# Kernel optimization log

Hardware: AMD Instinct MI355X
Metric: run time of the kernel (lower is better)

The kernel has to match this reference:

```python
import jax, jax.numpy as jnp
import numpy as np

B, T, ENC, TAG, HG, HE, M = 64, 383, 768, 128, 400, 256, 20
D = ENC + TAG          # graph RNN input size (encoder_output_dim + tag_representation_dim)
S = T + 1              # +1 for head sentinel


def setup_inputs() -> dict:
    ks = jax.random.split(jax.random.key(0), 16)
    g = lambda i, shape, s=0.05: jax.random.normal(ks[i], shape, dtype=jnp.float32) * s
    z = lambda n: jnp.zeros((n,), jnp.float32)
    return dict(
        input=g(0, (B, T, ENC), 1.0),
        tag_embeddings=g(1, (B, T, TAG), 1.0),
        mask=jnp.ones((B, T), jnp.int32),
        head_sentinel=g(2, (D,), 1.0),
        # bidirectional graph RNN (tanh, 1 layer)
        Wih_f=g(3, (HG, D)), Whh_f=g(4, (HG, HG)), bih_f=z(HG), bhh_f=z(HG),
        Wih_b=g(5, (HG, D)), Whh_b=g(6, (HG, HG)), bih_b=z(HG), bhh_b=z(HG),
        # graph_to_edge projection (edge RNN initial hidden)
        Wg2e=g(7, (HE, 2 * HG)), bg2e=z(HE),
        # edge RNN (past direction, input size 1) + edge classifier head
        Wih_e=g(8, (HE, 1)), Whh_e=g(9, (HE, HE)), bih_e=z(HE), bhh_e=z(HE),
        Wcls=g(10, (1, HE)), bcls=z(1),
        bos=z(1),
        # head/dep tag feedforwards
        Wht=g(11, (TAG, 2 * HG)), bht=z(TAG),
        Wdt=g(12, (TAG, 2 * HG)), bdt=z(TAG),
    )


def _masked_rnn(x, m, Wih, Whh, bih, bhh, reverse):
    # x: [B,S,D], m: [B,S,1]. Emulates packed nn.RNN(tanh) for one direction:
    # hidden only advances on valid steps (so the backward direction starts its
    # recurrence at each sequence's true length), outputs are zero on padding
    # (matching pad_packed_sequence zero padding).
    def step(h, inp):
        xt, mt = inp
        hn = jnp.tanh(xt @ Wih.T + bih + h @ Whh.T + bhh)
        h = mt * hn + (1.0 - mt) * h
        return h, h * mt

    h0 = jnp.zeros((x.shape[0], Wih.shape[0]), x.dtype)
    _, ys = jax.lax.scan(step, h0, (x.swapaxes(0, 1), m.swapaxes(0, 1)), reverse=reverse)
    return ys.swapaxes(0, 1)


def reference(input, tag_embeddings, mask, head_sentinel,
              Wih_f, Whh_f, bih_f, bhh_f, Wih_b, Whh_b, bih_b, bhh_b,
              Wg2e, bg2e, Wih_e, Whh_e, bih_e, bhh_e, Wcls, bcls, bos,
              Wht, bht, Wdt, bdt):
    x = jnp.concatenate([input, tag_embeddings], axis=-1)            # [B,T,D]
    sent = jnp.broadcast_to(head_sentinel, (B, 1, D))
    x = jnp.concatenate([sent, x], axis=1)                           # [B,S,D]
    m = jnp.concatenate([jnp.ones((B, 1), mask.dtype), mask], axis=1)  # sentinel is valid
    mf = m.astype(x.dtype)[..., None]                                # [B,S,1]

    fwd = _masked_rnn(x, mf, Wih_f, Whh_f, bih_f, bhh_f, reverse=False)
    bwd = _masked_rnn(x, mf, Wih_b, Whh_b, bih_b, bhh_b, reverse=True)
    graph_state = jnp.concatenate([fwd, bwd], axis=-1)               # [B,S,2*HG]

    # initial hidden = graph_to_edge(graph_state), input starts at bos, then
    # feeds back the previous logit.
    proj = graph_state.reshape(B * S, 2 * HG) @ Wg2e.T + bg2e        # [B*S,HE]
    steps = min(M, S)
    x0 = jnp.broadcast_to(bos.reshape(1, 1), (B * S, 1))

    def estep(carry, _):
        xe, h = carry
        hn = jnp.tanh(xe @ Wih_e.T + bih_e + h @ Whh_e.T + bhh_e)
        logit = hn @ Wcls.T + bcls                                   # [B*S,1]
        return (logit, hn), logit

    _, logits = jax.lax.scan(estep, (x0, proj), None, length=steps)  # [steps,B*S,1]
    Ap = logits.squeeze(-1).T.reshape(B, S, steps)                   # [B,S,steps]

    # banded scatter: arc_logits[:, i, start:i] = Ap[:, i, :i-start], start=max(0,i-M)
    rows = jnp.arange(S)[:, None]
    cols = jnp.arange(S)[None, :]
    start = jnp.maximum(0, rows - M)
    k = cols - start
    valid = (cols >= start) & (cols < rows)
    idx = jnp.clip(k, 0, steps - 1)
    band = Ap[:, jnp.broadcast_to(rows, (S, S)), jnp.broadcast_to(idx, (S, S))]  # [B,S,S]
    arc_logits = jnp.where(valid[None], band, jnp.zeros((), Ap.dtype))

    # tag feedforwards (Dropout is identity in eval)
    head_tag = jax.nn.elu(graph_state @ Wht.T + bht)
    dep_tag = jax.nn.elu(graph_state @ Wdt.T + bdt)
    return head_tag, dep_tag, arc_logits
```

## Files before the change

kernel.cpp:

```cpp
#include <hip/hip_runtime.h>

#define B_ 64
#define T_ 383
#define S_ 384
#define ENC_ 768
#define TAGD_ 128
#define D_ 896
#define HG_ 400
#define HE_ 256
#define MSTEP_ 20
#define RTOT_ (B_*S_)
#define HEAD_SZ_ ((size_t)RTOT_*TAGD_)

typedef short short8 __attribute__((ext_vector_type(8)));
typedef float f32x4 __attribute__((ext_vector_type(4)));

__device__ __forceinline__ float bf2f(unsigned short u){
  union { unsigned int i; float f; } v; v.i = ((unsigned int)u) << 16; return v.f;
}
__device__ __forceinline__ unsigned short f2bf(float f){
  union { float f; unsigned int i; } v; v.f = f;
  unsigned int r = (v.i + 0x7fffu + ((v.i >> 16) & 1u)) >> 16;
  return (unsigned short)r;
}
__device__ __forceinline__ float tanh_fast(float x){
  float xc = fminf(fmaxf(x, -15.f), 15.f);
  float e = __expf(2.f*xc);
  return (e - 1.f) * __builtin_amdgcn_rcpf(e + 1.f);
}

__device__ __forceinline__ void probe_maps(int lane, int* mlab, int* nlab){
  unsigned short lb = f2bf((float)(lane & 15));
  short8 av, bv;
  #pragma unroll
  for (int j = 0; j < 8; j++){ av[j] = (short)lb; bv[j] = (short)0x3F80; }
  f32x4 z = {0.f,0.f,0.f,0.f};
  f32x4 d1 = __builtin_amdgcn_mfma_f32_16x16x32_bf16(av, bv, z, 0, 0, 0);
  f32x4 d2 = __builtin_amdgcn_mfma_f32_16x16x32_bf16(bv, av, z, 0, 0, 0);
  #pragma unroll
  for (int i = 0; i < 4; i++){
    mlab[i] = (int)(d1[i]*0.03125f + 0.5f);
    nlab[i] = (int)(d2[i]*0.03125f + 0.5f);
  }
}

__global__ __launch_bounds__(256) void cvt4(const float* __restrict__ src,
                                            unsigned short* __restrict__ dst, int n4)
{
  int i = blockIdx.x*256 + threadIdx.x;
  if (i >= n4) return;
  float4 v = ((const float4*)src)[i];
  ((ushort4*)dst)[i] = make_ushort4(f2bf(v.x), f2bf(v.y), f2bf(v.z), f2bf(v.w));
}

__global__ __launch_bounds__(256) void pack_wrnn3(const float* __restrict__ Wf,
                                                  const float* __restrict__ Wb,
                                                  unsigned short* __restrict__ Wr)
{
  int idx = blockIdx.x*256 + threadIdx.x;
  if (idx >= 2*26*13*16*32) return;
  int dir = idx / (26*13*16*32);
  int rem = idx % (26*13*16*32);
  int tile = rem / (13*16*32); rem %= (13*16*32);
  int kt = rem / (16*32);      rem %= (16*32);
  int r  = rem / 32;
  int kk = rem % 32;
  int n = tile*16 + r, k = kt*32 + kk;
  unsigned short v = 0;
  if (n < HG_ && k < HG_) v = f2bf((dir ? Wb : Wf)[(size_t)n*HG_ + k]);
  Wr[idx] = v;
}

__global__ __launch_bounds__(64) void maskpack(const int* __restrict__ mask,
                                               unsigned long long* __restrict__ mb)
{
  int t = blockIdx.x; int b = threadIdx.x;
  int m = (t > 0) ? mask[b*T_ + (t-1)] : 1;
  unsigned long long v = __ballot(m != 0);
  if (b == 0) mb[t] = v;
}

__global__ __launch_bounds__(256) void gemm_pre(
    const float* __restrict__ inp, const float* __restrict__ tag,
    const float* __restrict__ sent, const unsigned short* __restrict__ W,
    const float* __restrict__ bihf, const float* __restrict__ bhhf,
    const float* __restrict__ bihb, const float* __restrict__ bhhb,
    unsigned short* __restrict__ preT2)
{
  int wid = blockIdx.x*4 + (threadIdx.x >> 6);
  int lane = threadIdx.x & 63;
  int q = lane >> 4, l16 = lane & 15;
  int mt = wid / 25, ct = wid % 25;
  int r = mt*16 + l16;
  int s = r % S_, b = r / S_;
  int mlab[4], nlab[4];
  probe_maps(lane, mlab, nlab);
  int n0 = ct*32 + l16, n1 = n0 + 16;
  const unsigned short* w0 = W + (size_t)n0*D_;
  const unsigned short* w1 = W + (size_t)n1*D_;
  f32x4 acc0 = {0.f,0.f,0.f,0.f}, acc1 = {0.f,0.f,0.f,0.f};
  for (int k0 = 0; k0 < D_; k0 += 32){
    int k = k0 + q*8;
    const float* asrc = (s == 0) ? (sent + k)
        : ((k < ENC_) ? inp + (size_t)(b*T_ + (s-1))*ENC_ + k
                      : tag + (size_t)(b*T_ + (s-1))*TAGD_ + (k - ENC_));
    float4 v0 = *(const float4*)asrc;
    float4 v1 = *(const float4*)(asrc + 4);
    union { unsigned int u[4]; short8 s8; } au;
    asm("v_cvt_pk_bf16_f32 %0, %1, %2" : "=v"(au.u[0]) : "v"(v0.x), "v"(v0.y));
    asm("v_cvt_pk_bf16_f32 %0, %1, %2" : "=v"(au.u[1]) : "v"(v0.z), "v"(v0.w));
    asm("v_cvt_pk_bf16_f32 %0, %1, %2" : "=v"(au.u[2]) : "v"(v1.x), "v"(v1.y));
    asm("v_cvt_pk_bf16_f32 %0, %1, %2" : "=v"(au.u[3]) : "v"(v1.z), "v"(v1.w));
    short8 a = au.s8;
    acc0 = __builtin_amdgcn_mfma_f32_16x16x32_bf16(a, *(const short8*)(w0 + k), acc0, 0,0,0);
    acc1 = __builtin_amdgcn_mfma_f32_16x16x32_bf16(a, *(const short8*)(w1 + k), acc1, 0,0,0);
  }
  #pragma unroll
  for (int i = 0; i < 4; i++){
    int row = mt*16 + mlab[i];
    int c0 = ct*32 + nlab[i], c1 = c0 + 16;
    int bb = row / S_, ss = row % S_;
    int mtb = bb >> 4, qb = (bb >> 2) & 3, rib = bb & 3;
    float v0 = acc0[i] + ((c0 < HG_) ? (bihf[c0] + bhhf[c0]) : (bihb[c0-HG_] + bhhb[c0-HG_]));
    float v1 = acc1[i] + ((c1 < HG_) ? (bihf[c1] + bhhf[c1]) : (bihb[c1-HG_] + bhhb[c1-HG_]));
    {
      int d = (c0 >= HG_) ? 1 : 0; int nn = c0 - d*HG_;
      int nt = nn >> 4, lc = nn & 15;
      preT2[((((size_t)(d*S_ + ss)*25 + nt)*4 + mtb)*64 + (qb*16 + lc))*4 + rib] = f2bf(v0);
    }
    {
      int d = (c1 >= HG_) ? 1 : 0; int nn = c1 - d*HG_;
      int nt = nn >> 4, lc = nn & 15;
      preT2[((((size_t)(d*S_ + ss)*25 + nt)*4 + mtb)*64 + (qb*16 + lc))*4 + rib] = f2bf(v1);
    }
  }
}

#define HSTR5_ 424
__device__ __forceinline__ void rnn_epi6(int n, const f32x4& acc, const ushort4& pu,
    unsigned long long mb, bool allm, int bg, int q,
    unsigned short (*Hh)[HSTR5_], unsigned short (*Hl)[HSTR5_])
{
  unsigned short pv[4] = {pu.x, pu.y, pu.z, pu.w};
  #pragma unroll
  for (int ri = 0; ri < 4; ri++){
    int b = q*4 + ri;
    float hn = tanh_fast(acc[ri] + bf2f(pv[ri]));
    float hnew;
    if (allm) hnew = hn;
    else {
      bool mv = (mb >> (bg*16 + b)) & 1ull;
      float hold = bf2f(Hh[b][n]) + bf2f(Hl[b][n]);
      hnew = mv ? hn : hold;
    }
    unsigned short hi = f2bf(hnew);
    Hh[b][n] = hi;
    Hl[b][n] = f2bf(hnew - bf2f(hi));
  }
}

template<bool EXTRA>
__device__ void rnn_body6(int nt0, int dir, int bg, int lane, int tid,
    const unsigned short* __restrict__ pD,
    const unsigned short* __restrict__ Wd,
    const unsigned long long* __restrict__ mbits,
    unsigned short* __restrict__ gs,
    unsigned short (*Hh)[HSTR5_], unsigned short (*Hl)[HSTR5_])
{
  int q = lane >> 4, l16 = lane & 15;

  short8 bh[3][13];
  #pragma unroll
  for (int j = 0; j < 3; j++){
    const unsigned short* wr = Wd + (size_t)(nt0 + j)*13*512 + l16*32 + q*8;
    #pragma unroll
    for (int kt = 0; kt < 13; kt++)
      bh[j][kt] = *(const short8*)(wr + kt*512);
  }
  const unsigned short* wx = Wd + (size_t)24*13*512 + l16*32 + q*8;

  for (int stp = 0; stp < S_; stp++){
    int t = dir ? (S_ - 1 - stp) : stp;
    unsigned long long mb = mbits[t];
    bool allm = (mb == 0xFFFFFFFFFFFFFFFFull);
    const unsigned short* pT = pD + (size_t)t*25600;

    ushort4 pu[3]; ushort4 pux = make_ushort4(0,0,0,0);
    #pragma unroll
    for (int j = 0; j < 3; j++)
      pu[j] = *(const ushort4*)(pT + (((size_t)(nt0 + j)*4 + bg)*64 + lane)*4);
    if (EXTRA)
      pux = *(const ushort4*)(pT + (((size_t)24*4 + bg)*64 + lane)*4);

    f32x4 acc[3]; f32x4 accx = {0.f,0.f,0.f,0.f};
    #pragma unroll
    for (int j = 0; j < 3; j++) acc[j] = (f32x4){0.f,0.f,0.f,0.f};

    #pragma unroll
    for (int kt = 0; kt < 13; kt++){
      short8 ah = *(const short8*)&Hh[l16][kt*32 + q*8];
      short8 al = *(const short8*)&Hl[l16][kt*32 + q*8];
      if (EXTRA){
        short8 bx = *(const short8*)(wx + kt*512);
        accx = __builtin_amdgcn_mfma_f32_16x16x32_bf16(ah, bx, accx, 0,0,0);
        accx = __builtin_amdgcn_mfma_f32_16x16x32_bf16(al, bx, accx, 0,0,0);
      }
      #pragma unroll
      for (int j = 0; j < 3; j++){
        acc[j] = __builtin_amdgcn_mfma_f32_16x16x32_bf16(ah, bh[j][kt], acc[j], 0,0,0);
        acc[j] = __builtin_amdgcn_mfma_f32_16x16x32_bf16(al, bh[j][kt], acc[j], 0,0,0);
      }
    }

    __syncthreads();

    #pragma unroll
    for (int j = 0; j < 3; j++)
      rnn_epi6((nt0 + j)*16 + l16, acc[j], pu[j], mb, allm, bg, q, Hh, Hl);
    if (EXTRA)
      rnn_epi6(24*16 + l16, accx, pux, mb, allm, bg, q, Hh, Hl);

    __syncthreads();

    for (int c = tid; c < 800; c += 512){
      int b = c / 50, off = c - b*50;
      uint4 dv = *(const uint4*)&Hh[b][off*8];
      bool mv = (mb >> (bg*16 + b)) & 1ull;
      uint4 z = make_uint4(0,0,0,0);
      *(uint4*)(gs + (size_t)((bg*16 + b)*S_ + t)*800 + dir*HG_ + off*8) = mv ? dv : z;
    }
  }
}

__global__ __launch_bounds__(512, 1) void rnn_mfma6(
    const unsigned short* __restrict__ preT2, const unsigned short* __restrict__ Wr,
    const unsigned long long* __restrict__ mbits, unsigned short* __restrict__ gs)
{
  __shared__ __align__(16) unsigned short Hh[16][HSTR5_];
  __shared__ __align__(16) unsigned short Hl[16][HSTR5_];
  int tid = threadIdx.x;
  int wave = tid >> 6, lane = tid & 63;
  int dir = blockIdx.x >> 2, bg = blockIdx.x & 3;
  for (int i = tid; i < 16*HSTR5_/2; i += 512){
    ((unsigned int*)Hh)[i] = 0u;
    ((unsigned int*)Hl)[i] = 0u;
  }
  __syncthreads();
  const unsigned short* Wd = Wr + (size_t)dir*26*13*512;
  const unsigned short* pD = preT2 + (size_t)dir*S_*25600;
  if (wave == 0) rnn_body6<true >(0,       dir, bg, lane, tid, pD, Wd, mbits, gs, Hh, Hl);
  else           rnn_body6<false>(wave*3,  dir, bg, lane, tid, pD, Wd, mbits, gs, Hh, Hl);
}

__global__ __launch_bounds__(256) void gemm_proj(
    const unsigned short* __restrict__ gs, const unsigned short* __restrict__ Wg2e,
    const float* __restrict__ bg2e, float* __restrict__ proj)
{
  int wid = blockIdx.x*4 + (threadIdx.x >> 6);
  int lane = threadIdx.x & 63;
  int q = lane >> 4, l16 = lane & 15;
  int mt = wid >> 3, ct = wid & 7;
  int mlab[4], nlab[4];
  probe_maps(lane, mlab, nlab);
  const unsigned short* arow = gs + (size_t)(mt*16 + l16)*800;
  int n0 = ct*32 + l16, n1 = n0 + 16;
  const unsigned short* w0 = Wg2e + (size_t)n0*800;
  const unsigned short* w1 = Wg2e + (size_t)n1*800;
  f32x4 acc0 = {0.f,0.f,0.f,0.f}, acc1 = {0.f,0.f,0.f,0.f};
  for (int k0 = 0; k0 < 800; k0 += 32){
    int k = k0 + q*8;
    short8 a = *(const short8*)(arow + k);
    acc0 = __builtin_amdgcn_mfma_f32_16x16x32_bf16(a, *(const short8*)(w0 + k), acc0, 0,0,0);
    acc1 = __builtin_amdgcn_mfma_f32_16x16x32_bf16(a, *(const short8*)(w1 + k), acc1, 0,0,0);
  }
  #pragma unroll
  for (int i = 0; i < 4; i++){
    int row = mt*16 + mlab[i];
    int c0 = ct*32 + nlab[i], c1 = c0 + 16;
    proj[(size_t)row*HE_ + c0] = acc0[i] + bg2e[c0];
    proj[(size_t)row*HE_ + c1] = acc1[i] + bg2e[c1];
  }
}

__global__ __launch_bounds__(256) void gemm_tag(
    const unsigned short* __restrict__ gs, const unsigned short* __restrict__ Wtag,
    const float* __restrict__ bht, const float* __restrict__ bdt,
    float* __restrict__ outH)
{
  int wid = blockIdx.x*4 + (threadIdx.x >> 6);
  int lane = threadIdx.x & 63;
  int q = lane >> 4, l16 = lane & 15;
  int mt = wid >> 3, ct = wid & 7;
  int mlab[4], nlab[4];
  probe_maps(lane, mlab, nlab);
  const unsigned short* arow = gs + (size_t)(mt*16 + l16)*800;
  int n0 = ct*32 + l16, n1 = n0 + 16;
  const unsigned short* w0 = Wtag + (size_t)n0*800;
  const unsigned short* w1 = Wtag + (size_t)n1*800;
  f32x4 acc0 = {0.f,0.f,0.f,0.f}, acc1 = {0.f,0.f,0.f,0.f};
  for (int k0 = 0; k0 < 800; k0 += 32){
    int k = k0 + q*8;
    short8 a = *(const short8*)(arow + k);
    acc0 = __builtin_amdgcn_mfma_f32_16x16x32_bf16(a, *(const short8*)(w0 + k), acc0, 0,0,0);
    acc1 = __builtin_amdgcn_mfma_f32_16x16x32_bf16(a, *(const short8*)(w1 + k), acc1, 0,0,0);
  }
  #pragma unroll
  for (int i = 0; i < 4; i++){
    int row = mt*16 + mlab[i];
    int c0 = ct*32 + nlab[i], c1 = c0 + 16;
    float v0 = acc0[i] + ((c0 < TAGD_) ? bht[c0] : bdt[c0-TAGD_]);
    float v1 = acc1[i] + ((c1 < TAGD_) ? bht[c1] : bdt[c1-TAGD_]);
    v0 = (v0 > 0.f) ? v0 : expm1f(v0);
    v1 = (v1 > 0.f) ? v1 : expm1f(v1);
    if (c0 < TAGD_) outH[(size_t)row*TAGD_ + c0] = v0;
    else            outH[HEAD_SZ_ + (size_t)row*TAGD_ + (c0-TAGD_)] = v0;
    if (c1 < TAGD_) outH[(size_t)row*TAGD_ + c1] = v1;
    else            outH[HEAD_SZ_ + (size_t)row*TAGD_ + (c1-TAGD_)] = v1;
  }
}

#define EROWS_ 96
#define ESTR_ 264
__global__ __launch_bounds__(256, 1) void estep2(
    const float* __restrict__ proj, const unsigned short* __restrict__ WhhE,
    const float* __restrict__ bihE, const float* __restrict__ bhhE,
    const float* __restrict__ WihE, const float* __restrict__ Wcls,
    const float* __restrict__ bclsp, const float* __restrict__ bosp,
    float* __restrict__ Ap)
{
  __shared__ __align__(16) unsigned short H[2][EROWS_][ESTR_];
  __shared__ float lacc[4][EROWS_];
  __shared__ float xls[EROWS_];
  int tid = threadIdx.x;
  int wave = tid >> 6, lane = tid & 63, q = lane >> 4, l16 = lane & 15;
  size_t rowbase = (size_t)blockIdx.x * EROWS_;

  short8 bw[4][8];
  float bias_n[4], wcl_n[4], wih_n[4];
  #pragma unroll
  for (int nt = 0; nt < 4; nt++){
    int n = wave*64 + nt*16 + l16;
    #pragma unroll
    for (int kt = 0; kt < 8; kt++)
      bw[nt][kt] = *(const short8*)(WhhE + (size_t)n*HE_ + kt*32 + q*8);
    bias_n[nt] = bihE[n] + bhhE[n];
    wcl_n[nt]  = Wcls[n];
    wih_n[nt]  = WihE[n];
  }
  for (int i = tid; i < EROWS_*HE_; i += 256){
    int r = i >> 8, n = i & 255;
    H[0][r][n] = f2bf(proj[(rowbase + r)*HE_ + n]);
  }
  if (tid < EROWS_) xls[tid] = bosp[0];
  float bc = bclsp[0];
  __syncthreads();

  for (int stp = 0; stp < MSTEP_; stp++){
    int cur = stp & 1, nxt = cur ^ 1;
    float lp[6][4];
    #pragma unroll
    for (int mt = 0; mt < 6; mt++){
      short8 af[8];
      #pragma unroll
      for (int kt = 0; kt < 8; kt++)
        af[kt] = *(const short8*)&H[cur][mt*16 + l16][kt*32 + q*8];
      float xr[4];
      #pragma unroll
      for (int ri = 0; ri < 4; ri++) xr[ri] = xls[mt*16 + q*4 + ri];
      f32x4 acc[4];
      #pragma unroll
      for (int nt = 0; nt < 4; nt++) acc[nt] = (f32x4){0.f,0.f,0.f,0.f};
      #pragma unroll
      for (int kt = 0; kt < 8; kt++){
        #pragma unroll
        for (int nt = 0; nt < 4; nt++)
          acc[nt] = __builtin_amdgcn_mfma_f32_16x16x32_bf16(af[kt], bw[nt][kt], acc[nt], 0,0,0);
      }
      #pragma unroll
      for (int ri = 0; ri < 4; ri++) lp[mt][ri] = 0.f;
      #pragma unroll
      for (int nt = 0; nt < 4; nt++){
        int n = wave*64 + nt*16 + l16;
        #pragma unroll
        for (int ri = 0; ri < 4; ri++){
          float v = acc[nt][ri] + bias_n[nt] + xr[ri]*wih_n[nt];
          float h = tanh_fast(v);
          lp[mt][ri] += h * wcl_n[nt];
          H[nxt][mt*16 + q*4 + ri][n] = f2bf(h);
        }
      }
    }
    #pragma unroll
    for (int mt = 0; mt < 6; mt++){
      #pragma unroll
      for (int ri = 0; ri < 4; ri++){
        float v = lp[mt][ri];
        v += __shfl_xor(v, 1, 16);
        v += __shfl_xor(v, 2, 16);
        v += __shfl_xor(v, 4, 16);
        v += __shfl_xor(v, 8, 16);
        lp[mt][ri] = v;
      }
    }
    if (l16 == 0){
      #pragma unroll
      for (int mt = 0; mt < 6; mt++)
        #pragma unroll
        for (int ri = 0; ri < 4; ri++)
          lacc[wave][mt*16 + q*4 + ri] = lp[mt][ri];
    }
    __syncthreads();
    if (tid < EROWS_){
      float lg = lacc[0][tid] + lacc[1][tid] + lacc[2][tid] + lacc[3][tid] + bc;
      Ap[(rowbase + tid)*MSTEP_ + stp] = lg;
      xls[tid] = lg;
    }
    __syncthreads();
  }
}

__global__ __launch_bounds__(256) void band_kernel(const float* __restrict__ Ap,
                                                   float* __restrict__ arc)
{
  int idx = blockIdx.x*256 + threadIdx.x;
  int c = idx % S_;
  int rr = (idx / S_) % S_;
  int b = idx / (S_*S_);
  int start = rr - MSTEP_; if (start < 0) start = 0;
  bool valid = (c >= start) && (c < rr);
  float v = 0.f;
  if (valid) v = Ap[(size_t)(b*S_ + rr)*MSTEP_ + (c - start)];
  arc[idx] = v;
}

extern "C" void kernel_launch(void* const* d_in, const int* in_sizes, int n_in,
                              void* d_out, int out_size, void* d_ws, size_t ws_size,
                              hipStream_t stream)
{
  const float* inp  = (const float*)d_in[0];
  const float* tag  = (const float*)d_in[1];
  const int*   mask = (const int*)d_in[2];
  const float* sent = (const float*)d_in[3];
  const float* Wihf = (const float*)d_in[4];
  const float* Whhf = (const float*)d_in[5];
  const float* bihf = (const float*)d_in[6];
  const float* bhhf = (const float*)d_in[7];
  const float* Wihb = (const float*)d_in[8];
  const float* Whhb = (const float*)d_in[9];
  const float* bihb = (const float*)d_in[10];
  const float* bhhb = (const float*)d_in[11];
  const float* Wg2e = (const float*)d_in[12];
  const float* bg2e = (const float*)d_in[13];
  const float* WihE = (const float*)d_in[14];
  const float* WhhE = (const float*)d_in[15];
  const float* bihE = (const float*)d_in[16];
  const float* bhhE = (const float*)d_in[17];
  const float* Wcls = (const float*)d_in[18];
  const float* bcls = (const float*)d_in[19];
  const float* bos  = (const float*)d_in[20];
  const float* Wht  = (const float*)d_in[21];
  const float* bht  = (const float*)d_in[22];
  const float* Wdt  = (const float*)d_in[23];
  const float* bdt  = (const float*)d_in[24];
  (void)in_sizes; (void)n_in; (void)out_size; (void)ws_size;

  char* ws = (char*)d_ws;
  unsigned short* preT2  = (unsigned short*)ws;
  unsigned short* gs     = (unsigned short*)(ws + 39321600);
  unsigned short* Wrnn3  = (unsigned short*)(ws + 78643200);
  unsigned short* Wihcat = (unsigned short*)(ws + 79335424);
  unsigned short* Wg2e_b = (unsigned short*)(ws + 80769024);
  unsigned short* Wtag_b = (unsigned short*)(ws + 81178624);
  unsigned short* WhhE_b = (unsigned short*)(ws + 81588224);
  unsigned long long* maskb = (unsigned long long*)(ws + 81719296);
  float*          proj   = (float*)ws;
  float*          Ap     = (float*)(ws + 25165824);

  float* outH   = (float*)d_out;
  float* outArc = outH + 2*HEAD_SZ_;

  hipLaunchKernelGGL(cvt4, dim3(350), dim3(256), 0, stream, Wihf, Wihcat,           400*896/4);
  hipLaunchKernelGGL(cvt4, dim3(350), dim3(256), 0, stream, Wihb, Wihcat + 400*896, 400*896/4);
  hipLaunchKernelGGL(cvt4, dim3(200), dim3(256), 0, stream, Wg2e, Wg2e_b,           256*800/4);
  hipLaunchKernelGGL(cvt4, dim3(100), dim3(256), 0, stream, Wht,  Wtag_b,           128*800/4);
  hipLaunchKernelGGL(cvt4, dim3(100), dim3(256), 0, stream, Wdt,  Wtag_b + 128*800, 128*800/4);
  hipLaunchKernelGGL(cvt4, dim3(64),  dim3(256), 0, stream, WhhE, WhhE_b,           256*256/4);
  hipLaunchKernelGGL(pack_wrnn3, dim3(1352), dim3(256), 0, stream, Whhf, Whhb, Wrnn3);
  hipLaunchKernelGGL(maskpack, dim3(S_), dim3(64), 0, stream, mask, maskb);
  hipLaunchKernelGGL(gemm_pre, dim3(9600), dim3(256), 0, stream,
                     inp, tag, sent, Wihcat, bihf, bhhf, bihb, bhhb, preT2);
  hipLaunchKernelGGL(rnn_mfma6, dim3(8), dim3(512), 0, stream, preT2, Wrnn3, maskb, gs);
  hipLaunchKernelGGL(gemm_proj, dim3(3072), dim3(256), 0, stream, gs, Wg2e_b, bg2e, proj);
  hipLaunchKernelGGL(gemm_tag,  dim3(3072), dim3(256), 0, stream, gs, Wtag_b, bht, bdt, outH);
  hipLaunchKernelGGL(estep2, dim3(256), dim3(256), 0, stream,
                     proj, WhhE_b, bihE, bhhE, WihE, Wcls, bcls, bos, Ap);
  hipLaunchKernelGGL(band_kernel, dim3(36864), dim3(256), 0, stream, Ap, outArc);
}
```

Baseline: 2.313 ms.

## Double-buffer RNN hidden state and halve waves holding weights in AGPRs

The sequential RNN kernel now runs 4 waves per block instead of 8, each owning 6 column tiles, with recurrent weights split between AGPRs and VGPRs through inline-asm register constraints. The hidden state is double-buffered in shared memory, so the epilogue writes the next buffer directly and one of the two per-step barriers is removed. This targets barrier and cross-wave synchronisation cost on the latency-bound recurrence, at the price of more MFMA work per wave and less parallelism per step.

```diff
diff --git a/kernel.cpp b/kernel.cpp
--- a/kernel.cpp
+++ b/kernel.cpp
@@ -136,10 +136,11 @@
   }
 }
 
-#define HSTR5_ 424
-__device__ __forceinline__ void rnn_epi6(int n, const f32x4& acc, const ushort4& pu,
+#define HSTR7_ 424
+__device__ __forceinline__ void rnn_epi7(int n, int x16, int c16,
+    const f32x4& acc, const ushort4& pu,
     unsigned long long mb, bool allm, int bg, int q,
-    unsigned short (*Hh)[HSTR5_], unsigned short (*Hl)[HSTR5_])
+    unsigned short (*Hh)[HSTR7_], unsigned short (*Hl)[HSTR7_])
 {
   unsigned short pv[4] = {pu.x, pu.y, pu.z, pu.w};
   #pragma unroll
@@ -150,106 +151,128 @@
     if (allm) hnew = hn;
     else {
       bool mv = (mb >> (bg*16 + b)) & 1ull;
-      float hold = bf2f(Hh[b][n]) + bf2f(Hl[b][n]);
+      float hold = bf2f(Hh[c16 + b][n]) + bf2f(Hl[c16 + b][n]);
       hnew = mv ? hn : hold;
     }
     unsigned short hi = f2bf(hnew);
-    Hh[b][n] = hi;
-    Hl[b][n] = f2bf(hnew - bf2f(hi));
+    Hh[x16 + b][n] = hi;
+    Hl[x16 + b][n] = f2bf(hnew - bf2f(hi));
   }
 }
 
 template<bool EXTRA>
-__device__ void rnn_body6(int nt0, int dir, int bg, int lane, int tid,
+__device__ void rnn_body7(int nt0, int dir, int bg, int lane, int tid,
     const unsigned short* __restrict__ pD,
     const unsigned short* __restrict__ Wd,
     const unsigned long long* __restrict__ mbits,
     unsigned short* __restrict__ gs,
-    unsigned short (*Hh)[HSTR5_], unsigned short (*Hl)[HSTR5_])
+    unsigned short (*Hh)[HSTR7_], unsigned short (*Hl)[HSTR7_])
 {
   int q = lane >> 4, l16 = lane & 15;
 
-  short8 bh[3][13];
-  #pragma unroll
-  for (int j = 0; j < 3; j++){
+  short8 bhA[4][13], bhV[2][13];
+  #pragma unroll
+  for (int j = 0; j < 4; j++){
     const unsigned short* wr = Wd + (size_t)(nt0 + j)*13*512 + l16*32 + q*8;
     #pragma unroll
-    for (int kt = 0; kt < 13; kt++)
-      bh[j][kt] = *(const short8*)(wr + kt*512);
-  }
+    for (int kt = 0; kt < 13; kt++) bhA[j][kt] = *(const short8*)(wr + kt*512);
+  }
+  #pragma unroll
+  for (int j = 0; j < 2; j++){
+    const unsigned short* wr = Wd + (size_t)(nt0 + 4 + j)*13*512 + l16*32 + q*8;
+    #pragma unroll
+    for (int kt = 0; kt < 13; kt++) bhV[j][kt] = *(const short8*)(wr + kt*512);
+  }
+  #pragma unroll
+  for (int j = 0; j < 4; j++)
+    #pragma unroll
+    for (int kt = 0; kt < 13; kt++) asm volatile("" : "+a"(bhA[j][kt]));
+  #pragma unroll
+  for (int j = 0; j < 2; j++)
+    #pragma unroll
+    for (int kt = 0; kt < 13; kt++) asm volatile("" : "+v"(bhV[j][kt]));
+
   const unsigned short* wx = Wd + (size_t)24*13*512 + l16*32 + q*8;
 
+  int cur = 0;
   for (int stp = 0; stp < S_; stp++){
     int t = dir ? (S_ - 1 - stp) : stp;
     unsigned long long mb = mbits[t];
     bool allm = (mb == 0xFFFFFFFFFFFFFFFFull);
     const unsigned short* pT = pD + (size_t)t*25600;
-
-    ushort4 pu[3]; ushort4 pux = make_ushort4(0,0,0,0);
-    #pragma unroll
-    for (int j = 0; j < 3; j++)
+    int c16 = cur*16, x16 = 16 - c16;
+
+    ushort4 pu[6]; ushort4 pux = make_ushort4(0,0,0,0);
+    #pragma unroll
+    for (int j = 0; j < 6; j++)
       pu[j] = *(const ushort4*)(pT + (((size_t)(nt0 + j)*4 + bg)*64 + lane)*4);
     if (EXTRA)
       pux = *(const ushort4*)(pT + (((size_t)24*4 + bg)*64 + lane)*4);
 
-    f32x4 acc[3]; f32x4 accx = {0.f,0.f,0.f,0.f};
-    #pragma unroll
-    for (int j = 0; j < 3; j++) acc[j] = (f32x4){0.f,0.f,0.f,0.f};
+    f32x4 acc[6]; f32x4 accx = {0.f,0.f,0.f,0.f};
+    #pragma unroll
+    for (int j = 0; j < 6; j++) acc[j] = (f32x4){0.f,0.f,0.f,0.f};
 
     #pragma unroll
     for (int kt = 0; kt < 13; kt++){
-      short8 ah = *(const short8*)&Hh[l16][kt*32 + q*8];
-      short8 al = *(const short8*)&Hl[l16][kt*32 + q*8];
+      short8 ah = *(const short8*)&Hh[c16 + l16][kt*32 + q*8];
+      short8 al = *(const short8*)&Hl[c16 + l16][kt*32 + q*8];
       if (EXTRA){
         short8 bx = *(const short8*)(wx + kt*512);
         accx = __builtin_amdgcn_mfma_f32_16x16x32_bf16(ah, bx, accx, 0,0,0);
         accx = __builtin_amdgcn_mfma_f32_16x16x32_bf16(al, bx, accx, 0,0,0);
       }
       #pragma unroll
-      for (int j = 0; j < 3; j++){
-        acc[j] = __builtin_amdgcn_mfma_f32_16x16x32_bf16(ah, bh[j][kt], acc[j], 0,0,0);
-        acc[j] = __builtin_amdgcn_mfma_f32_16x16x32_bf16(al, bh[j][kt], acc[j], 0,0,0);
+      for (int j = 0; j < 4; j++){
+        acc[j] = __builtin_amdgcn_mfma_f32_16x16x32_bf16(ah, bhA[j][kt], acc[j], 0,0,0);
+        acc[j] = __builtin_amdgcn_mfma_f32_16x16x32_bf16(al, bhA[j][kt], acc[j], 0,0,0);
       }
-    }
+      #pragma unroll
+      for (int j = 0; j < 2; j++){
+        acc[4+j] = __builtin_amdgcn_mfma_f32_16x16x32_bf16(ah, bhV[j][kt], acc[4+j], 0,0,0);
+        acc[4+j] = __builtin_amdgcn_mfma_f32_16x16x32_bf16(al, bhV[j][kt], acc[4+j], 0,0,0);
+      }
+    }
+
+    #pragma unroll
+    for (int j = 0; j < 6; j++)
+      rnn_epi7((nt0 + j)*16 + l16, x16, c16, acc[j], pu[j], mb, allm, bg, q, Hh, Hl);
+    if (EXTRA)
+      rnn_epi7(24*16 + l16, x16, c16, accx, pux, mb, allm, bg, q, Hh, Hl);
 
     __syncthreads();
 
-    #pragma unroll
-    for (int j = 0; j < 3; j++)
-      rnn_epi6((nt0 + j)*16 + l16, acc[j], pu[j], mb, allm, bg, q, Hh, Hl);
-    if (EXTRA)
-      rnn_epi6(24*16 + l16, accx, pux, mb, allm, bg, q, Hh, Hl);
-
-    __syncthreads();
-
-    for (int c = tid; c < 800; c += 512){
+    for (int c = tid; c < 800; c += 256){
       int b = c / 50, off = c - b*50;
-      uint4 dv = *(const uint4*)&Hh[b][off*8];
+      uint4 dv = *(const uint4*)&Hh[x16 + b][off*8];
       bool mv = (mb >> (bg*16 + b)) & 1ull;
       uint4 z = make_uint4(0,0,0,0);
       *(uint4*)(gs + (size_t)((bg*16 + b)*S_ + t)*800 + dir*HG_ + off*8) = mv ? dv : z;
     }
-  }
-}
-
-__global__ __launch_bounds__(512, 1) void rnn_mfma6(
+    cur ^= 1;
+  }
+}
+
+__global__ __launch_bounds__(256)
+__attribute__((amdgpu_waves_per_eu(1, 1)))
+void rnn_mfma7(
     const unsigned short* __restrict__ preT2, const unsigned short* __restrict__ Wr,
     const unsigned long long* __restrict__ mbits, unsigned short* __restrict__ gs)
 {
-  __shared__ __align__(16) unsigned short Hh[16][HSTR5_];
-  __shared__ __align__(16) unsigned short Hl[16][HSTR5_];
+  __shared__ __align__(16) unsigned short Hh[32][HSTR7_];
+  __shared__ __align__(16) unsigned short Hl[32][HSTR7_];
   int tid = threadIdx.x;
   int wave = tid >> 6, lane = tid & 63;
   int dir = blockIdx.x >> 2, bg = blockIdx.x & 3;
-  for (int i = tid; i < 16*HSTR5_/2; i += 512){
+  for (int i = tid; i < 32*HSTR7_/2; i += 256){
     ((unsigned int*)Hh)[i] = 0u;
     ((unsigned int*)Hl)[i] = 0u;
   }
   __syncthreads();
   const unsigned short* Wd = Wr + (size_t)dir*26*13*512;
   const unsigned short* pD = preT2 + (size_t)dir*S_*25600;
-  if (wave == 0) rnn_body6<true >(0,       dir, bg, lane, tid, pD, Wd, mbits, gs, Hh, Hl);
-  else           rnn_body6<false>(wave*3,  dir, bg, lane, tid, pD, Wd, mbits, gs, Hh, Hl);
+  if (wave == 0) rnn_body7<true >(0,       dir, bg, lane, tid, pD, Wd, mbits, gs, Hh, Hl);
+  else           rnn_body7<false>(wave*6,  dir, bg, lane, tid, pD, Wd, mbits, gs, Hh, Hl);
 }
 
 __global__ __launch_bounds__(256) void gemm_proj(
@@ -489,7 +512,7 @@
   hipLaunchKernelGGL(maskpack, dim3(S_), dim3(64), 0, stream, mask, maskb);
   hipLaunchKernelGGL(gemm_pre, dim3(9600), dim3(256), 0, stream,
                      inp, tag, sent, Wihcat, bihf, bhhf, bihb, bhhb, preT2);
-  hipLaunchKernelGGL(rnn_mfma6, dim3(8), dim3(512), 0, stream, preT2, Wrnn3, maskb, gs);
+  hipLaunchKernelGGL(rnn_mfma7, dim3(8), dim3(256), 0, stream, preT2, Wrnn3, maskb, gs);
   hipLaunchKernelGGL(gemm_proj, dim3(3072), dim3(256), 0, stream, gs, Wg2e_b, bg2e, proj);
   hipLaunchKernelGGL(gemm_tag,  dim3(3072), dim3(256), 0, stream, gs, Wtag_b, bht, bdt, outH);
   hipLaunchKernelGGL(estep2, dim3(256), dim3(256), 0, stream,
```

New measurement: 2.697 ms. 16.6% more time.

## Double-buffer RNN hidden state in LDS to remove one barrier per step

Applied to the files above, without the earlier changes.

The recurrent kernel now keeps two copies of the hidden-state buffers in shared memory. Each step reads from the current buffer and writes to the other, so the barrier between the MFMA reads and the epilogue writes is dropped, leaving one __syncthreads per timestep on the serial critical path. It also pins the weight registers with empty asm constraints and swaps the launch bound for a waves-per-EU attribute to steer register allocation. The cost is double the LDS for the hidden state and some risk of register spills.

```diff
diff --git a/kernel.cpp b/kernel.cpp
--- a/kernel.cpp
+++ b/kernel.cpp
@@ -136,10 +136,11 @@
   }
 }
 
-#define HSTR5_ 424
-__device__ __forceinline__ void rnn_epi6(int n, const f32x4& acc, const ushort4& pu,
+#define HSTR7_ 424
+__device__ __forceinline__ void rnn_epi8(int n, int x16, int c16,
+    const f32x4& acc, const ushort4& pu,
     unsigned long long mb, bool allm, int bg, int q,
-    unsigned short (*Hh)[HSTR5_], unsigned short (*Hl)[HSTR5_])
+    unsigned short (*Hh)[HSTR7_], unsigned short (*Hl)[HSTR7_])
 {
   unsigned short pv[4] = {pu.x, pu.y, pu.z, pu.w};
   #pragma unroll
@@ -150,22 +151,22 @@
     if (allm) hnew = hn;
     else {
       bool mv = (mb >> (bg*16 + b)) & 1ull;
-      float hold = bf2f(Hh[b][n]) + bf2f(Hl[b][n]);
+      float hold = bf2f(Hh[c16 + b][n]) + bf2f(Hl[c16 + b][n]);
       hnew = mv ? hn : hold;
     }
     unsigned short hi = f2bf(hnew);
-    Hh[b][n] = hi;
-    Hl[b][n] = f2bf(hnew - bf2f(hi));
+    Hh[x16 + b][n] = hi;
+    Hl[x16 + b][n] = f2bf(hnew - bf2f(hi));
   }
 }
 
 template<bool EXTRA>
-__device__ void rnn_body6(int nt0, int dir, int bg, int lane, int tid,
+__device__ void rnn_body8(int nt0, int dir, int bg, int lane, int tid,
     const unsigned short* __restrict__ pD,
     const unsigned short* __restrict__ Wd,
     const unsigned long long* __restrict__ mbits,
     unsigned short* __restrict__ gs,
-    unsigned short (*Hh)[HSTR5_], unsigned short (*Hl)[HSTR5_])
+    unsigned short (*Hh)[HSTR7_], unsigned short (*Hl)[HSTR7_])
 {
   int q = lane >> 4, l16 = lane & 15;
 
@@ -174,16 +175,22 @@
   for (int j = 0; j < 3; j++){
     const unsigned short* wr = Wd + (size_t)(nt0 + j)*13*512 + l16*32 + q*8;
     #pragma unroll
-    for (int kt = 0; kt < 13; kt++)
-      bh[j][kt] = *(const short8*)(wr + kt*512);
-  }
+    for (int kt = 0; kt < 13; kt++) bh[j][kt] = *(const short8*)(wr + kt*512);
+  }
+  #pragma unroll
+  for (int j = 0; j < 3; j++)
+    #pragma unroll
+    for (int kt = 0; kt < 13; kt++) asm volatile("" : "+v"(bh[j][kt]));
+
   const unsigned short* wx = Wd + (size_t)24*13*512 + l16*32 + q*8;
 
+  int cur = 0;
   for (int stp = 0; stp < S_; stp++){
     int t = dir ? (S_ - 1 - stp) : stp;
     unsigned long long mb = mbits[t];
     bool allm = (mb == 0xFFFFFFFFFFFFFFFFull);
     const unsigned short* pT = pD + (size_t)t*25600;
+    int c16 = cur*16, x16 = 16 - c16;
 
     ushort4 pu[3]; ushort4 pux = make_ushort4(0,0,0,0);
     #pragma unroll
@@ -198,8 +205,8 @@
 
     #pragma unroll
     for (int kt = 0; kt < 13; kt++){
-      short8 ah = *(const short8*)&Hh[l16][kt*32 + q*8];
-      short8 al = *(const short8*)&Hl[l16][kt*32 + q*8];
+      short8 ah = *(const short8*)&Hh[c16 + l16][kt*32 + q*8];
+      short8 al = *(const short8*)&Hl[c16 + l16][kt*32 + q*8];
       if (EXTRA){
         short8 bx = *(const short8*)(wx + kt*512);
         accx = __builtin_amdgcn_mfma_f32_16x16x32_bf16(ah, bx, accx, 0,0,0);
@@ -212,44 +219,45 @@
       }
     }
 
-    __syncthreads();
-
     #pragma unroll
     for (int j = 0; j < 3; j++)
-      rnn_epi6((nt0 + j)*16 + l16, acc[j], pu[j], mb, allm, bg, q, Hh, Hl);
+      rnn_epi8((nt0 + j)*16 + l16, x16, c16, acc[j], pu[j], mb, allm, bg, q, Hh, Hl);
     if (EXTRA)
-      rnn_epi6(24*16 + l16, accx, pux, mb, allm, bg, q, Hh, Hl);
+      rnn_epi8(24*16 + l16, x16, c16, accx, pux, mb, allm, bg, q, Hh, Hl);
 
     __syncthreads();
 
     for (int c = tid; c < 800; c += 512){
       int b = c / 50, off = c - b*50;
-      uint4 dv = *(const uint4*)&Hh[b][off*8];
+      uint4 dv = *(const uint4*)&Hh[x16 + b][off*8];
       bool mv = (mb >> (bg*16 + b)) & 1ull;
       uint4 z = make_uint4(0,0,0,0);
       *(uint4*)(gs + (size_t)((bg*16 + b)*S_ + t)*800 + dir*HG_ + off*8) = mv ? dv : z;
     }
-  }
-}
-
-__global__ __launch_bounds__(512, 1) void rnn_mfma6(
+    cur ^= 1;
+  }
+}
+
+__global__ __launch_bounds__(512)
+__attribute__((amdgpu_waves_per_eu(2, 2)))
+void rnn_mfma8(
     const unsigned short* __restrict__ preT2, const unsigned short* __restrict__ Wr,
     const unsigned long long* __restrict__ mbits, unsigned short* __restrict__ gs)
 {
-  __shared__ __align__(16) unsigned short Hh[16][HSTR5_];
-  __shared__ __align__(16) unsigned short Hl[16][HSTR5_];
+  __shared__ __align__(16) unsigned short Hh[32][HSTR7_];
+  __shared__ __align__(16) unsigned short Hl[32][HSTR7_];
   int tid = threadIdx.x;
   int wave = tid >> 6, lane = tid & 63;
   int dir = blockIdx.x >> 2, bg = blockIdx.x & 3;
-  for (int i = tid; i < 16*HSTR5_/2; i += 512){
+  for (int i = tid; i < 32*HSTR7_/2; i += 512){
     ((unsigned int*)Hh)[i] = 0u;
     ((unsigned int*)Hl)[i] = 0u;
   }
   __syncthreads();
   const unsigned short* Wd = Wr + (size_t)dir*26*13*512;
   const unsigned short* pD = preT2 + (size_t)dir*S_*25600;
-  if (wave == 0) rnn_body6<true >(0,       dir, bg, lane, tid, pD, Wd, mbits, gs, Hh, Hl);
-  else           rnn_body6<false>(wave*3,  dir, bg, lane, tid, pD, Wd, mbits, gs, Hh, Hl);
+  if (wave == 0) rnn_body8<true >(0,       dir, bg, lane, tid, pD, Wd, mbits, gs, Hh, Hl);
+  else           rnn_body8<false>(wave*3,  dir, bg, lane, tid, pD, Wd, mbits, gs, Hh, Hl);
 }
 
 __global__ __launch_bounds__(256) void gemm_proj(
@@ -489,7 +497,7 @@
   hipLaunchKernelGGL(maskpack, dim3(S_), dim3(64), 0, stream, mask, maskb);
   hipLaunchKernelGGL(gemm_pre, dim3(9600), dim3(256), 0, stream,
                      inp, tag, sent, Wihcat, bihf, bhhf, bihb, bhhb, preT2);
-  hipLaunchKernelGGL(rnn_mfma6, dim3(8), dim3(512), 0, stream, preT2, Wrnn3, maskb, gs);
+  hipLaunchKernelGGL(rnn_mfma8, dim3(8), dim3(512), 0, stream, preT2, Wrnn3, maskb, gs);
   hipLaunchKernelGGL(gemm_proj, dim3(3072), dim3(256), 0, stream, gs, Wg2e_b, bg2e, proj);
   hipLaunchKernelGGL(gemm_tag,  dim3(3072), dim3(256), 0, stream, gs, Wtag_b, bht, bdt, outH);
   hipLaunchKernelGGL(estep2, dim3(256), dim3(256), 0, stream,
```

Measured after the change: 2.452 ms. 6.0% more time.
